# Kernel optimization log

Hardware: AMD Instinct MI355X
Metric: run time of the kernel (lower is better)

## Reference

```python
import jax, jax.numpy as jnp
import numpy as np

NDIM = 1024
NHEAD = 16
B, T = 4, 2048
EPS = 1e-05
GELU_C = np.sqrt(2.0 / np.pi).astype(np.float32)


def new_gelu(x):
    return 0.5 * x * (1.0 + jnp.tanh(GELU_C * (x + 0.044715 * x ** 3)))


def layer_norm(x, w, b):
    mu = jnp.mean(x, axis=-1, keepdims=True)
    var = jnp.var(x, axis=-1, keepdims=True)
    return (x - mu) * jax.lax.rsqrt(var + EPS) * w + b


def setup_inputs() -> dict:
    key = jax.random.key(0)
    ks = jax.random.split(key, 8)
    d, dff = NDIM, 4 * NDIM
    s = 0.02
    return {
        "x": jax.random.normal(ks[0], (B, T, d), jnp.float32),
        "ln1_w": jnp.ones((d,), jnp.float32),
        "ln1_b": jnp.zeros((d,), jnp.float32),
        "w_attn": jax.random.normal(ks[1], (d, 3 * d), jnp.float32) * s,
        "b_attn": jnp.zeros((3 * d,), jnp.float32),
        "w_proj": jax.random.normal(ks[2], (d, d), jnp.float32) * s,
        "b_proj": jnp.zeros((d,), jnp.float32),
        "ln2_w": jnp.ones((d,), jnp.float32),
        "ln2_b": jnp.zeros((d,), jnp.float32),
        "w_fc": jax.random.normal(ks[3], (d, dff), jnp.float32) * s,
        "b_fc": jnp.zeros((dff,), jnp.float32),
        "w_fc2": jax.random.normal(ks[4], (dff, d), jnp.float32) * s,
        "b_fc2": jnp.zeros((d,), jnp.float32),
    }


def reference(x, ln1_w, ln1_b, w_attn, b_attn, w_proj, b_proj,
              ln2_w, ln2_b, w_fc, b_fc, w_fc2, b_fc2):
    Bx, Tx, C = x.shape
    hd = C // NHEAD
    # --- attention ---
    h = layer_norm(x, ln1_w, ln1_b)
    qkv = h @ w_attn + b_attn                       # [B,T,3C]
    q, k, v = jnp.split(qkv, 3, axis=-1)
    q = q.reshape(Bx, Tx, NHEAD, hd).transpose(0, 2, 1, 3)  # [B,H,T,hd]
    k = k.reshape(Bx, Tx, NHEAD, hd).transpose(0, 2, 1, 3)
    v = v.reshape(Bx, Tx, NHEAD, hd).transpose(0, 2, 1, 3)
    att = jnp.einsum('bhqd,bhkd->bhqk', q, k) * (1.0 / np.sqrt(hd).astype(np.float32))
    causal = jnp.tril(jnp.ones((Tx, Tx), bool))
    att = jnp.where(causal[None, None], att, jnp.float32(-jnp.inf))
    att = jax.nn.softmax(att, axis=-1)
    y = jnp.einsum('bhqk,bhkd->bhqd', att, v)
    y = y.transpose(0, 2, 1, 3).reshape(Bx, Tx, C)
    x = x + y @ w_proj + b_proj
    # --- MLP ---
    h2 = layer_norm(x, ln2_w, ln2_b)
    x = x + new_gelu(h2 @ w_fc + b_fc) @ w_fc2 + b_fc2
    return x
```

## Files before the change

kernel.cpp:

```cpp
#include <hip/hip_runtime.h>

typedef __attribute__((ext_vector_type(8))) short short8;
typedef __attribute__((ext_vector_type(8))) unsigned short ushort8;
typedef __attribute__((ext_vector_type(4))) float f32x4;
typedef __attribute__((ext_vector_type(16))) float f32x16;
typedef __attribute__((ext_vector_type(2))) unsigned int uint2v;
typedef unsigned int uint32;

__device__ __forceinline__ unsigned short f2bf(float f){
  union { float f; unsigned int u; } x; x.f = f;
  unsigned int u = x.u;
  u += 0x7fffu + ((u >> 16) & 1u);
  return (unsigned short)(u >> 16);
}
__device__ __forceinline__ float bf2f(unsigned short s){
  union { float f; unsigned int u; } x; x.u = ((uint32)s) << 16; return x.f;
}

typedef __attribute__((address_space(1))) void gvoid;
typedef __attribute__((address_space(3))) void lvoid;
__device__ __forceinline__ void gload_lds16(const void* g, void* l){
  __builtin_amdgcn_global_load_lds((gvoid*)g, (lvoid*)l, 16, 0, 0);
}

__device__ __forceinline__ f32x4 mfma_bf16(short8 a, short8 b, f32x4 c){
  return __builtin_amdgcn_mfma_f32_16x16x32_bf16(a, b, c, 0, 0, 0);
}
__device__ __forceinline__ f32x16 mfma32(short8 a, short8 b, f32x16 c){
  return __builtin_amdgcn_mfma_f32_32x32x16_bf16(a, b, c, 0, 0, 0);
}

__device__ __forceinline__ uint32 cvtpk_bf(float lo, float hi){
  uint32 r;
  asm("v_cvt_pk_bf16_f32 %0, %1, %2" : "=v"(r) : "v"(lo), "v"(hi));
  return r;
}
__device__ __forceinline__ void plswap(uint32& a, uint32& b){
  auto r = __builtin_amdgcn_permlane32_swap(a, b, false, false);
  a = r[0]; b = r[1];
}

#if __has_builtin(__builtin_amdgcn_exp2f)
__device__ __forceinline__ float exp2g(float x){ return __builtin_amdgcn_exp2f(x); }
#else
__device__ __forceinline__ float exp2g(float x){ return exp2f(x); }
#endif

__device__ __forceinline__ f32x16 zero16(){
  f32x16 z;
  #pragma unroll
  for (int i = 0; i < 16; i++) z[i] = 0.0f;
  return z;
}

__global__ __launch_bounds__(256) void wtrans_kernel(
    const float* __restrict__ w, unsigned short* __restrict__ wt, int K, int N)
{
  __shared__ float tile[32][33];
  const int n0 = blockIdx.x * 32;
  const int k0 = blockIdx.y * 32;
  const int t = threadIdx.x;
  #pragma unroll
  for (int i = 0; i < 4; i++){
    const int e = t + i * 256;
    const int r = e >> 5, c = e & 31;
    tile[r][c] = w[(size_t)(k0 + r) * N + n0 + c];
  }
  __syncthreads();
  #pragma unroll
  for (int i = 0; i < 4; i++){
    const int e = t + i * 256;
    const int r = e >> 5, c = e & 31;
    wt[(size_t)(n0 + r) * K + k0 + c] = f2bf(tile[c][r]);
  }
}

__global__ __launch_bounds__(256) void vtrans_kernel(
    const unsigned short* __restrict__ qkv, unsigned short* __restrict__ vt)
{
  __shared__ unsigned short tile[32][33];
  const int bh = blockIdx.z;
  const int b = bh >> 4, h = bh & 15;
  const int t0 = blockIdx.x * 32;
  const int f0 = blockIdx.y * 32;
  const int t = threadIdx.x;
  #pragma unroll
  for (int i = 0; i < 4; i++){
    const int e = t + i * 256;
    const int r = e >> 5, c = e & 31;
    tile[r][c] = qkv[(size_t)(b * 2048 + t0 + r) * 3072 + 2048 + h * 64 + f0 + c];
  }
  __syncthreads();
  #pragma unroll
  for (int i = 0; i < 4; i++){
    const int e = t + i * 256;
    const int r = e >> 5, c = e & 31;
    vt[((size_t)bh * 64 + f0 + r) * 2048 + t0 + c] = tile[c][r];
  }
}

__global__ __launch_bounds__(256) void ln_kernel(
    const float* __restrict__ x, const float* __restrict__ w, const float* __restrict__ b,
    unsigned short* __restrict__ out)
{
  const int row = blockIdx.x;
  const int t = threadIdx.x;
  const float4 v = ((const float4*)(x + (size_t)row * 1024))[t];
  float s  = v.x + v.y + v.z + v.w;
  float s2 = v.x * v.x + v.y * v.y + v.z * v.z + v.w * v.w;
  #pragma unroll
  for (int off = 32; off > 0; off >>= 1){
    s  += __shfl_xor(s, off);
    s2 += __shfl_xor(s2, off);
  }
  __shared__ float ps[8];
  const int wid = t >> 6;
  if ((t & 63) == 0){ ps[wid] = s; ps[4 + wid] = s2; }
  __syncthreads();
  s  = ps[0] + ps[1] + ps[2] + ps[3];
  s2 = ps[4] + ps[5] + ps[6] + ps[7];
  const float mu  = s * (1.0f / 1024.0f);
  const float var = s2 * (1.0f / 1024.0f) - mu * mu;
  const float rs  = rsqrtf(var + 1e-5f);
  const float4 wv = ((const float4*)w)[t];
  const float4 bv = ((const float4*)b)[t];
  ushort4 ov;
  ov.x = f2bf((v.x - mu) * rs * wv.x + bv.x);
  ov.y = f2bf((v.y - mu) * rs * wv.y + bv.y);
  ov.z = f2bf((v.z - mu) * rs * wv.z + bv.z);
  ov.w = f2bf((v.w - mu) * rs * wv.w + bv.w);
  ((ushort4*)(out + (size_t)row * 1024))[t] = ov;
}

#define EPI_BF16   0
#define EPI_RESF32 1
#define EPI_GELU   2

template<int EPI, int BN>
__global__ __launch_bounds__(512, 2) void gemm3_kernel(
    const unsigned short* __restrict__ A,
    const unsigned short* __restrict__ BT,
    const float* __restrict__ bias,
    const float* __restrict__ res,
    void* __restrict__ outp,
    int M, int N, int K)
{
  constexpr int NJ   = BN / 64;
  constexpr int BSL  = BN * 64;
  constexpr int SBUF = 32768 + 2 * BSL;
  constexpr int NBL  = BN / 128;
  __shared__ __align__(16) char lds[2 * SBUF];

  const int nwg = gridDim.x;
  const int bid = blockIdx.x;
  const int wg = (bid & 7) * (nwg >> 3) + (bid >> 3);
  const int NTile = N / BN;
  const int mt = wg / NTile;
  const int nti = wg - mt * NTile;
  const int m0 = mt << 8;
  const int n0 = nti * BN;

  const int tid = threadIdx.x;
  const int lane = tid & 63;
  const int wid = tid >> 6;
  const int wv_m = wid >> 2;
  const int wv_n = wid & 3;
  const int fr = lane & 15;
  const int fg = lane >> 4;

  const unsigned short* aSrc[2];
  int aDst[2];
  #pragma unroll
  for (int l = 0; l < 2; l++){
    const int s = l * 512 + tid;
    const int r = s >> 2, c = s & 3;
    aSrc[l] = A + (size_t)(m0 + r) * K + ((c ^ ((r >> 1) & 3)) << 3);
    aDst[l] = s * 16;
  }
  const unsigned short* bSrc[2];
  int bDst[2];
  #pragma unroll
  for (int l = 0; l < NBL; l++){
    const int s = l * 512 + tid;
    const int r = s >> 2, c = s & 3;
    bSrc[l] = BT + (size_t)(n0 + r) * K + ((c ^ ((r >> 1) & 3)) << 3);
    bDst[l] = 32768 + s * 16;
  }

  int aOff[8], bOff[NJ];
  #pragma unroll
  for (int mi = 0; mi < 8; mi++){
    const int row = wv_m * 128 + mi * 16 + fr;
    aOff[mi] = row * 64 + ((fg ^ ((row >> 1) & 3)) << 4);
  }
  #pragma unroll
  for (int nj = 0; nj < NJ; nj++){
    const int row = wv_n * (BN / 4) + nj * 16 + fr;
    bOff[nj] = 32768 + row * 64 + ((fg ^ ((row >> 1) & 3)) << 4);
  }

  f32x4 acc[8][NJ];
  #pragma unroll
  for (int i = 0; i < 8; i++)
    #pragma unroll
    for (int j = 0; j < NJ; j++) acc[i][j] = (f32x4){0.f, 0.f, 0.f, 0.f};

#define STAGE(tt, kss, bufc) do { \
    const size_t ko = (size_t)(tt) * 64 + (kss) * 32; \
    gload_lds16(aSrc[0] + ko, lds + (bufc) + (kss) * 16384 + aDst[0]); \
    gload_lds16(aSrc[1] + ko, lds + (bufc) + (kss) * 16384 + aDst[1]); \
    gload_lds16(bSrc[0] + ko, lds + (bufc) + (kss) * BSL + bDst[0]); \
    if (NBL == 2) gload_lds16(bSrc[1] + ko, lds + (bufc) + (kss) * BSL + bDst[1]); \
  } while (0)

  const int nt = K >> 6;

  STAGE(0, 0, 0);
  STAGE(0, 1, 0);
  if (BN == 256) asm volatile("s_waitcnt vmcnt(4)" ::: "memory");
  else           asm volatile("s_waitcnt vmcnt(3)" ::: "memory");
  __builtin_amdgcn_s_barrier();

  int bufc = 0;
  for (int t = 0; t < nt; t++){
    const int obuf = bufc ^ SBUF;
    const bool pf = (t + 1 < nt);
    #pragma unroll
    for (int ks = 0; ks < 2; ks++){
      short8 aF[8], bF[NJ];
      #pragma unroll
      for (int mi = 0; mi < 8; mi++)
        aF[mi] = *(const short8*)(lds + bufc + ks * 16384 + aOff[mi]);
      #pragma unroll
      for (int nj = 0; nj < NJ; nj++)
        bF[nj] = *(const short8*)(lds + bufc + ks * BSL + bOff[nj]);
      if (pf) STAGE(t + 1, ks, obuf);
      __builtin_amdgcn_s_barrier();
      asm volatile("s_waitcnt lgkmcnt(0)" ::: "memory");
      __builtin_amdgcn_sched_barrier(0);
      __builtin_amdgcn_s_setprio(1);
      #pragma unroll
      for (int mi = 0; mi < 8; mi++)
        #pragma unroll
        for (int nj = 0; nj < NJ; nj++)
          acc[mi][nj] = mfma_bf16(aF[mi], bF[nj], acc[mi][nj]);
      __builtin_amdgcn_s_setprio(0);
      if (pf){
        if (BN == 256) asm volatile("s_waitcnt vmcnt(4)" ::: "memory");
        else           asm volatile("s_waitcnt vmcnt(3)" ::: "memory");
      } else if (ks == 0){
        asm volatile("s_waitcnt vmcnt(0)" ::: "memory");
      }
      __builtin_amdgcn_s_barrier();
    }
    bufc ^= SBUF;
  }
#undef STAGE

  #pragma unroll
  for (int mi = 0; mi < 8; mi++){
    const int mrow = m0 + wv_m * 128 + mi * 16 + fg * 4;
    #pragma unroll
    for (int nj = 0; nj < NJ; nj++){
      const int ncol = n0 + wv_n * (BN / 4) + nj * 16 + fr;
      const float bv = bias[ncol];
      #pragma unroll
      for (int r2 = 0; r2 < 4; r2++){
        const size_t idx = (size_t)(mrow + r2) * N + ncol;
        float v = acc[mi][nj][r2] + bv;
        if (EPI == EPI_RESF32){
          ((float*)outp)[idx] = v + res[idx];
        } else if (EPI == EPI_GELU){
          const float tt = tanhf(0.7978845608028654f * (v + 0.044715f * v * v * v));
          ((unsigned short*)outp)[idx] = f2bf(0.5f * v * (1.0f + tt));
        } else {
          ((unsigned short*)outp)[idx] = f2bf(v);
        }
      }
    }
  }
}

template<bool MASK>
__device__ __forceinline__ void attn_tile(
    const unsigned short* __restrict__ Kc, const unsigned short* __restrict__ Vc,
    const short8 (&qf)[4], int kvbase, int qg, int l31, int hi,
    float& m_r, float& lsum, f32x16& Oa, f32x16& Ob)
{
  f32x16 Sa = zero16();
  f32x16 Sb = zero16();
  const int xb = l31 & 7;
  #pragma unroll
  for (int kk = 0; kk < 4; kk++){
    const int x = kk * 2 + hi;
    const short8 k0 = *(const short8*)((const char*)Kc + l31 * 128 + ((x ^ xb) << 4));
    const short8 k1 = *(const short8*)((const char*)Kc + (l31 + 32) * 128 + ((x ^ xb) << 4));
    Sa = mfma32(k0, qf[kk], Sa);
    Sb = mfma32(k1, qf[kk], Sb);
  }
  if (MASK){
    #pragma unroll
    for (int r = 0; r < 16; r++){
      const int kva = kvbase + (r & 3) + 8 * (r >> 2) + 4 * hi;
      Sa[r] = (kva > qg)      ? -1e30f : Sa[r];
      Sb[r] = (kva + 32 > qg) ? -1e30f : Sb[r];
    }
  }
  float tmax = Sa[0];
  #pragma unroll
  for (int r = 1; r < 16; r++) tmax = fmaxf(tmax, Sa[r]);
  #pragma unroll
  for (int r = 0; r < 16; r++) tmax = fmaxf(tmax, Sb[r]);
  tmax = fmaxf(tmax, __shfl_xor(tmax, 32));
  if (__any(tmax > m_r + 10.0f)){
    const float mn = fmaxf(m_r, tmax);
    const float sc = exp2g(m_r - mn);
    m_r = mn;
    lsum *= sc;
    #pragma unroll
    for (int r = 0; r < 16; r++){ Oa[r] *= sc; Ob[r] *= sc; }
  }
  float rs = 0.0f;
  #pragma unroll
  for (int r = 0; r < 16; r++){
    Sa[r] = exp2g(Sa[r] - m_r); rs += Sa[r];
    Sb[r] = exp2g(Sb[r] - m_r); rs += Sb[r];
  }
  rs += __shfl_xor(rs, 32);
  lsum += rs;

  short8 pf[4];
  {
    uint32 a0 = cvtpk_bf(Sa[0], Sa[1]),   b0 = cvtpk_bf(Sa[4], Sa[5]);
    uint32 a1 = cvtpk_bf(Sa[2], Sa[3]),   b1 = cvtpk_bf(Sa[6], Sa[7]);
    plswap(a0, b0); plswap(a1, b1);
    uint32 a2 = cvtpk_bf(Sa[8], Sa[9]),   b2 = cvtpk_bf(Sa[12], Sa[13]);
    uint32 a3 = cvtpk_bf(Sa[10], Sa[11]), b3 = cvtpk_bf(Sa[14], Sa[15]);
    plswap(a2, b2); plswap(a3, b3);
    union { uint32 u[4]; short8 s; } m0, m1;
    m0.u[0] = a0; m0.u[1] = a1; m0.u[2] = b0; m0.u[3] = b1;
    m1.u[0] = a2; m1.u[1] = a3; m1.u[2] = b2; m1.u[3] = b3;
    pf[0] = m0.s; pf[1] = m1.s;
  }
  {
    uint32 a0 = cvtpk_bf(Sb[0], Sb[1]),   b0 = cvtpk_bf(Sb[4], Sb[5]);
    uint32 a1 = cvtpk_bf(Sb[2], Sb[3]),   b1 = cvtpk_bf(Sb[6], Sb[7]);
    plswap(a0, b0); plswap(a1, b1);
    uint32 a2 = cvtpk_bf(Sb[8], Sb[9]),   b2 = cvtpk_bf(Sb[12], Sb[13]);
    uint32 a3 = cvtpk_bf(Sb[10], Sb[11]), b3 = cvtpk_bf(Sb[14], Sb[15]);
    plswap(a2, b2); plswap(a3, b3);
    union { uint32 u[4]; short8 s; } m0, m1;
    m0.u[0] = a0; m0.u[1] = a1; m0.u[2] = b0; m0.u[3] = b1;
    m1.u[0] = a2; m1.u[1] = a3; m1.u[2] = b2; m1.u[3] = b3;
    pf[2] = m0.s; pf[3] = m1.s;
  }
  #pragma unroll
  for (int kk = 0; kk < 4; kk++){
    const int x = kk * 2 + hi;
    const short8 v0 = *(const short8*)((const char*)Vc + l31 * 128 + ((x ^ xb) << 4));
    const short8 v1 = *(const short8*)((const char*)Vc + (l31 + 32) * 128 + ((x ^ xb) << 4));
    Oa = mfma32(v0, pf[kk], Oa);
    Ob = mfma32(v1, pf[kk], Ob);
  }
}

__global__ __launch_bounds__(256) void attn_kernel(
    const unsigned short* __restrict__ qkv,
    const unsigned short* __restrict__ vt,
    unsigned short* __restrict__ y)
{
  __shared__ __align__(16) unsigned short Klds[2][4096];
  __shared__ __align__(16) unsigned short Vlds[2][4096];
  const int bid = blockIdx.x;
  const int bh = bid & 63;
  const int qb_i = bid >> 6;
  const int b = bh >> 4, h = bh & 15;
  const int qb0 = qb_i * 128;
  const int tid = threadIdx.x;
  const int w = tid >> 6;
  const int lane = tid & 63;
  const int l31 = lane & 31;
  const int hi = lane >> 5;

  const int qrow_g = b * 2048 + qb0 + w * 32 + l31;
  const unsigned short* qp = qkv + (size_t)qrow_g * 3072 + h * 64;
  short8 qf[4];
  #pragma unroll
  for (int kk = 0; kk < 4; kk++){
    short8 raw = *(const short8*)&qp[kk * 16 + hi * 8];
    #pragma unroll
    for (int j = 0; j < 8; j++)
      qf[kk][j] = (short)f2bf(bf2f((unsigned short)raw[j]) * 0.18033688011112042f);
  }

  const int sr = tid >> 3;
  const int ce = ((tid & 7) ^ (sr & 7)) * 8;
  const unsigned short* kb = qkv + (size_t)(b * 2048) * 3072 + 1024 + h * 64;
  const unsigned short* vb = vt + (size_t)bh * 64 * 2048;

  f32x16 Oa = zero16(), Ob = zero16();
  float m_r = -1e30f, lsum = 0.0f;
  const int qmin = qb0 + w * 32;
  const int qmax = qmin + 31;
  const int qg = qmin + l31;
  const int nkv = (qb0 >> 6) + 2;

#define STAGE(t, bb) do { \
    const size_t kro = (size_t)((t) * 64 + sr) * 3072; \
    gload_lds16(kb + kro + ce,                         (char*)&Klds[bb][0] + tid * 16); \
    gload_lds16(kb + kro + (size_t)32 * 3072 + ce,     (char*)&Klds[bb][0] + 4096 + tid * 16); \
    gload_lds16(vb + (size_t)sr * 2048 + (t) * 64 + ce,        (char*)&Vlds[bb][0] + tid * 16); \
    gload_lds16(vb + (size_t)(sr + 32) * 2048 + (t) * 64 + ce, (char*)&Vlds[bb][0] + 4096 + tid * 16); \
  } while (0)

  STAGE(0, 0);
  __syncthreads();
  int cur = 0;
  for (int kvt = 0; kvt < nkv; kvt++){
    if (kvt + 1 < nkv){
      if (cur) STAGE(kvt + 1, 0); else STAGE(kvt + 1, 1);
    }
    if (kvt * 64 <= qmax){
      if (kvt * 64 + 63 <= qmin)
        attn_tile<false>(Klds[cur], Vlds[cur], qf, kvt * 64, qg, l31, hi, m_r, lsum, Oa, Ob);
      else
        attn_tile<true >(Klds[cur], Vlds[cur], qf, kvt * 64, qg, l31, hi, m_r, lsum, Oa, Ob);
    }
    __syncthreads();
    cur ^= 1;
  }
#undef STAGE

  const float inv = 1.0f / lsum;
  unsigned short* yp = y + (size_t)qrow_g * 1024 + h * 64;
  #pragma unroll
  for (int c2 = 0; c2 < 4; c2++){
    uint2v da, db;
    da.x = cvtpk_bf(Oa[4 * c2 + 0] * inv, Oa[4 * c2 + 1] * inv);
    da.y = cvtpk_bf(Oa[4 * c2 + 2] * inv, Oa[4 * c2 + 3] * inv);
    *(uint2v*)&yp[8 * c2 + 4 * hi] = da;
    db.x = cvtpk_bf(Ob[4 * c2 + 0] * inv, Ob[4 * c2 + 1] * inv);
    db.y = cvtpk_bf(Ob[4 * c2 + 2] * inv, Ob[4 * c2 + 3] * inv);
    *(uint2v*)&yp[32 + 8 * c2 + 4 * hi] = db;
  }
}

extern "C" void kernel_launch(void* const* d_in, const int* in_sizes, int n_in,
                              void* d_out, int out_size, void* d_ws, size_t ws_size,
                              hipStream_t stream)
{
  const float* x      = (const float*)d_in[0];
  const float* ln1_w  = (const float*)d_in[1];
  const float* ln1_b  = (const float*)d_in[2];
  const float* w_attn = (const float*)d_in[3];
  const float* b_attn = (const float*)d_in[4];
  const float* w_proj = (const float*)d_in[5];
  const float* b_proj = (const float*)d_in[6];
  const float* ln2_w  = (const float*)d_in[7];
  const float* ln2_b  = (const float*)d_in[8];
  const float* w_fc   = (const float*)d_in[9];
  const float* b_fc   = (const float*)d_in[10];
  const float* w_fc2  = (const float*)d_in[11];
  const float* b_fc2  = (const float*)d_in[12];

  char* ws = (char*)d_ws;
  unsigned short* wbT_attn = (unsigned short*)(ws + 0);
  unsigned short* wbT_proj = (unsigned short*)(ws + 6291456);
  unsigned short* wbT_fc   = (unsigned short*)(ws + 8388608);
  unsigned short* wbT_fc2  = (unsigned short*)(ws + 16777216);
  unsigned short* h_bf     = (unsigned short*)(ws + 25165824);
  unsigned short* qkv_bf   = (unsigned short*)(ws + 41943040);
  unsigned short* vt_bf    = (unsigned short*)(ws + 92274688);
  unsigned short* g_bf     = (unsigned short*)(ws + 41943040);
  unsigned short* y_bf     = (unsigned short*)(ws + 109051904);
  float*          x1       = (float*)(ws + 125829120);
  float* outf = (float*)d_out;

  wtrans_kernel<<<dim3(3072/32, 1024/32), 256, 0, stream>>>(w_attn, wbT_attn, 1024, 3072);
  wtrans_kernel<<<dim3(1024/32, 1024/32), 256, 0, stream>>>(w_proj, wbT_proj, 1024, 1024);
  wtrans_kernel<<<dim3(4096/32, 1024/32), 256, 0, stream>>>(w_fc,   wbT_fc,   1024, 4096);
  wtrans_kernel<<<dim3(1024/32, 4096/32), 256, 0, stream>>>(w_fc2,  wbT_fc2,  4096, 1024);

  ln_kernel<<<8192, 256, 0, stream>>>(x, ln1_w, ln1_b, h_bf);
  gemm3_kernel<EPI_BF16, 256><<<384, 512, 0, stream>>>(
      h_bf, wbT_attn, b_attn, nullptr, qkv_bf, 8192, 3072, 1024);
  vtrans_kernel<<<dim3(64, 2, 64), 256, 0, stream>>>(qkv_bf, vt_bf);
  attn_kernel<<<1024, 256, 0, stream>>>(qkv_bf, vt_bf, y_bf);
  gemm3_kernel<EPI_RESF32, 128><<<256, 512, 0, stream>>>(
      y_bf, wbT_proj, b_proj, x, x1, 8192, 1024, 1024);
  ln_kernel<<<8192, 256, 0, stream>>>(x1, ln2_w, ln2_b, h_bf);
  gemm3_kernel<EPI_GELU, 256><<<512, 512, 0, stream>>>(
      h_bf, wbT_fc, b_fc, nullptr, g_bf, 8192, 4096, 1024);
  gemm3_kernel<EPI_RESF32, 128><<<256, 512, 0, stream>>>(
      g_bf, wbT_fc2, b_fc2, x1, outf, 8192, 1024, 4096);
}
```

Baseline: 393.9 us.

## Restructure GEMM into 4-slot k-slice pipeline with split A/B staging

Replaces the double-buffered 64-wide K tile loop with a 4-slot ring of 32-wide K slices, prefetching three slices ahead with vmcnt waits tuned to the pipeline depth. For BN=128 the wave layout changes to 4x2 with 64-row wave tiles, and for BN=256 the MFMA work is split into two sub-phases that interleave A and B prefetch issue. The intent is to hide global load latency better and spread memory issue across compute phases. The cost is more barriers per K step and a different LDS footprint, which could hurt occupancy.

Result: no change. 392.5 us (-0.3%).

```diff
diff --git a/kernel.cpp b/kernel.cpp
--- a/kernel.cpp
+++ b/kernel.cpp
@@ -137,7 +137,7 @@
 #define EPI_GELU   2
 
 template<int EPI, int BN>
-__global__ __launch_bounds__(512, 2) void gemm3_kernel(
+__global__ __launch_bounds__(512, 2) void gemm4_kernel(
     const unsigned short* __restrict__ A,
     const unsigned short* __restrict__ BT,
     const float* __restrict__ bias,
@@ -145,11 +145,14 @@
     void* __restrict__ outp,
     int M, int N, int K)
 {
-  constexpr int NJ   = BN / 64;
-  constexpr int BSL  = BN * 64;
-  constexpr int SBUF = 32768 + 2 * BSL;
+  constexpr int MI   = (BN == 256) ? 8 : 4;
+  constexpr int SP   = MI / 4;
   constexpr int NBL  = BN / 128;
-  __shared__ __align__(16) char lds[2 * SBUF];
+  constexpr int WN   = (BN == 256) ? 4 : 2;
+  constexpr int WROWS= (BN == 256) ? 128 : 64;
+  constexpr int ASL  = 16384;
+  constexpr int SLOT = ASL + BN * 64;
+  __shared__ __align__(16) char lds[4 * SLOT];
 
   const int nwg = gridDim.x;
   const int bid = blockIdx.x;
@@ -163,8 +166,8 @@
   const int tid = threadIdx.x;
   const int lane = tid & 63;
   const int wid = tid >> 6;
-  const int wv_m = wid >> 2;
-  const int wv_n = wid & 3;
+  const int wv_m = wid / WN;
+  const int wv_n = wid % WN;
   const int fr = lane & 15;
   const int fg = lane >> 4;
 
@@ -177,92 +180,110 @@
     aSrc[l] = A + (size_t)(m0 + r) * K + ((c ^ ((r >> 1) & 3)) << 3);
     aDst[l] = s * 16;
   }
-  const unsigned short* bSrc[2];
-  int bDst[2];
+  const unsigned short* bSrc[NBL];
+  int bDst[NBL];
   #pragma unroll
   for (int l = 0; l < NBL; l++){
     const int s = l * 512 + tid;
     const int r = s >> 2, c = s & 3;
     bSrc[l] = BT + (size_t)(n0 + r) * K + ((c ^ ((r >> 1) & 3)) << 3);
-    bDst[l] = 32768 + s * 16;
-  }
-
-  int aOff[8], bOff[NJ];
-  #pragma unroll
-  for (int mi = 0; mi < 8; mi++){
-    const int row = wv_m * 128 + mi * 16 + fr;
+    bDst[l] = ASL + s * 16;
+  }
+
+  int aOff[MI], bOff[4];
+  #pragma unroll
+  for (int mi = 0; mi < MI; mi++){
+    const int row = wv_m * WROWS + mi * 16 + fr;
     aOff[mi] = row * 64 + ((fg ^ ((row >> 1) & 3)) << 4);
   }
   #pragma unroll
-  for (int nj = 0; nj < NJ; nj++){
-    const int row = wv_n * (BN / 4) + nj * 16 + fr;
-    bOff[nj] = 32768 + row * 64 + ((fg ^ ((row >> 1) & 3)) << 4);
-  }
-
-  f32x4 acc[8][NJ];
-  #pragma unroll
-  for (int i = 0; i < 8; i++)
+  for (int nj = 0; nj < 4; nj++){
+    const int row = wv_n * 64 + nj * 16 + fr;
+    bOff[nj] = ASL + row * 64 + ((fg ^ ((row >> 1) & 3)) << 4);
+  }
+
+  f32x4 acc[MI][4];
+  #pragma unroll
+  for (int i = 0; i < MI; i++)
     #pragma unroll
-    for (int j = 0; j < NJ; j++) acc[i][j] = (f32x4){0.f, 0.f, 0.f, 0.f};
-
-#define STAGE(tt, kss, bufc) do { \
-    const size_t ko = (size_t)(tt) * 64 + (kss) * 32; \
-    gload_lds16(aSrc[0] + ko, lds + (bufc) + (kss) * 16384 + aDst[0]); \
-    gload_lds16(aSrc[1] + ko, lds + (bufc) + (kss) * 16384 + aDst[1]); \
-    gload_lds16(bSrc[0] + ko, lds + (bufc) + (kss) * BSL + bDst[0]); \
-    if (NBL == 2) gload_lds16(bSrc[1] + ko, lds + (bufc) + (kss) * BSL + bDst[1]); \
+    for (int j = 0; j < 4; j++) acc[i][j] = (f32x4){0.f, 0.f, 0.f, 0.f};
+
+#define STAGE_A(sl, slot) do { \
+    gload_lds16(aSrc[0] + (size_t)(sl) * 32, lds + (slot) + aDst[0]); \
+    gload_lds16(aSrc[1] + (size_t)(sl) * 32, lds + (slot) + aDst[1]); \
   } while (0)
-
-  const int nt = K >> 6;
-
-  STAGE(0, 0, 0);
-  STAGE(0, 1, 0);
-  if (BN == 256) asm volatile("s_waitcnt vmcnt(4)" ::: "memory");
-  else           asm volatile("s_waitcnt vmcnt(3)" ::: "memory");
+#define STAGE_B(sl, slot) do { \
+    gload_lds16(bSrc[0] + (size_t)(sl) * 32, lds + (slot) + bDst[0]); \
+    if (NBL == 2) gload_lds16(bSrc[1] + (size_t)(sl) * 32, lds + (slot) + bDst[1]); \
+  } while (0)
+
+  const int NS = K >> 5;
+
+  STAGE_A(0, 0);        STAGE_B(0, 0);
+  STAGE_A(1, SLOT);     STAGE_B(1, SLOT);
+  STAGE_A(2, 2 * SLOT); STAGE_B(2, 2 * SLOT);
+  if (BN == 256) asm volatile("s_waitcnt vmcnt(8)" ::: "memory");
+  else           asm volatile("s_waitcnt vmcnt(6)" ::: "memory");
   __builtin_amdgcn_s_barrier();
 
-  int bufc = 0;
-  for (int t = 0; t < nt; t++){
-    const int obuf = bufc ^ SBUF;
-    const bool pf = (t + 1 < nt);
+  for (int s = 0; s < NS; s++){
+    const int ss = (s & 3) * SLOT;
+    const int sg = ((s + 3) & 3) * SLOT;
+    const bool pf = (s + 3 < NS);
+    short8 bF[4];
     #pragma unroll
-    for (int ks = 0; ks < 2; ks++){
-      short8 aF[8], bF[NJ];
+    for (int sp = 0; sp < SP; sp++){
+      short8 aF[4];
       #pragma unroll
-      for (int mi = 0; mi < 8; mi++)
-        aF[mi] = *(const short8*)(lds + bufc + ks * 16384 + aOff[mi]);
-      #pragma unroll
-      for (int nj = 0; nj < NJ; nj++)
-        bF[nj] = *(const short8*)(lds + bufc + ks * BSL + bOff[nj]);
-      if (pf) STAGE(t + 1, ks, obuf);
+      for (int i = 0; i < 4; i++)
+        aF[i] = *(const short8*)(lds + ss + aOff[sp * 4 + i]);
+      if (sp == 0){
+        #pragma unroll
+        for (int nj = 0; nj < 4; nj++)
+          bF[nj] = *(const short8*)(lds + ss + bOff[nj]);
+      }
+      if (pf){
+        if (SP == 2){
+          if (sp == 0) STAGE_A(s + 3, sg);
+          else         STAGE_B(s + 3, sg);
+        } else {
+          STAGE_A(s + 3, sg);
+          STAGE_B(s + 3, sg);
+        }
+      }
       __builtin_amdgcn_s_barrier();
       asm volatile("s_waitcnt lgkmcnt(0)" ::: "memory");
       __builtin_amdgcn_sched_barrier(0);
       __builtin_amdgcn_s_setprio(1);
       #pragma unroll
-      for (int mi = 0; mi < 8; mi++)
+      for (int i = 0; i < 4; i++)
         #pragma unroll
-        for (int nj = 0; nj < NJ; nj++)
-          acc[mi][nj] = mfma_bf16(aF[mi], bF[nj], acc[mi][nj]);
+        for (int nj = 0; nj < 4; nj++)
+          acc[sp * 4 + i][nj] = mfma_bf16(aF[i], bF[nj], acc[sp * 4 + i][nj]);
       __builtin_amdgcn_s_setprio(0);
-      if (pf){
-        if (BN == 256) asm volatile("s_waitcnt vmcnt(4)" ::: "memory");
-        else           asm volatile("s_waitcnt vmcnt(3)" ::: "memory");
-      } else if (ks == 0){
-        asm volatile("s_waitcnt vmcnt(0)" ::: "memory");
+      if (sp == SP - 1){
+        if (s + 3 < NS){
+          if (BN == 256) asm volatile("s_waitcnt vmcnt(8)" ::: "memory");
+          else           asm volatile("s_waitcnt vmcnt(6)" ::: "memory");
+        } else if (s + 2 < NS){
+          if (BN == 256) asm volatile("s_waitcnt vmcnt(4)" ::: "memory");
+          else           asm volatile("s_waitcnt vmcnt(3)" ::: "memory");
+        } else if (s + 1 < NS){
+          asm volatile("s_waitcnt vmcnt(0)" ::: "memory");
+        }
       }
       __builtin_amdgcn_s_barrier();
     }
-    bufc ^= SBUF;
-  }
-#undef STAGE
-
-  #pragma unroll
-  for (int mi = 0; mi < 8; mi++){
-    const int mrow = m0 + wv_m * 128 + mi * 16 + fg * 4;
+  }
+#undef STAGE_A
+#undef STAGE_B
+
+  #pragma unroll
+  for (int mi = 0; mi < MI; mi++){
+    const int mrow = m0 + wv_m * WROWS + mi * 16 + fg * 4;
     #pragma unroll
-    for (int nj = 0; nj < NJ; nj++){
-      const int ncol = n0 + wv_n * (BN / 4) + nj * 16 + fr;
+    for (int nj = 0; nj < 4; nj++){
+      const int ncol = n0 + wv_n * 64 + nj * 16 + fr;
       const float bv = bias[ncol];
       #pragma unroll
       for (int r2 = 0; r2 < 4; r2++){
@@ -482,15 +503,15 @@
   wtrans_kernel<<<dim3(1024/32, 4096/32), 256, 0, stream>>>(w_fc2,  wbT_fc2,  4096, 1024);
 
   ln_kernel<<<8192, 256, 0, stream>>>(x, ln1_w, ln1_b, h_bf);
-  gemm3_kernel<EPI_BF16, 256><<<384, 512, 0, stream>>>(
+  gemm4_kernel<EPI_BF16, 256><<<384, 512, 0, stream>>>(
       h_bf, wbT_attn, b_attn, nullptr, qkv_bf, 8192, 3072, 1024);
   vtrans_kernel<<<dim3(64, 2, 64), 256, 0, stream>>>(qkv_bf, vt_bf);
   attn_kernel<<<1024, 256, 0, stream>>>(qkv_bf, vt_bf, y_bf);
-  gemm3_kernel<EPI_RESF32, 128><<<256, 512, 0, stream>>>(
+  gemm4_kernel<EPI_RESF32, 128><<<256, 512, 0, stream>>>(
       y_bf, wbT_proj, b_proj, x, x1, 8192, 1024, 1024);
   ln_kernel<<<8192, 256, 0, stream>>>(x1, ln2_w, ln2_b, h_bf);
-  gemm3_kernel<EPI_GELU, 256><<<512, 512, 0, stream>>>(
+  gemm4_kernel<EPI_GELU, 256><<<512, 512, 0, stream>>>(
       h_bf, wbT_fc, b_fc, nullptr, g_bf, 8192, 4096, 1024);
-  gemm3_kernel<EPI_RESF32, 128><<<256, 512, 0, stream>>>(
+  gemm4_kernel<EPI_RESF32, 128><<<256, 512, 0, stream>>>(
       g_bf, wbT_fc2, b_fc2, x1, outf, 8192, 1024, 4096);
 }
```
